# Performance work log

Measured on AMD Instinct MI355X. Metric: run time of the kernel, lower is better.

The kernel has to match this reference:

```python
import jax, jax.numpy as jnp
import numpy as np

N, F, R, E, L = 100000, 128, 4, 1600000, 2


def setup_inputs() -> dict:
    key = jax.random.key(0)
    k1, k2, k3, k4, k5 = jax.random.split(key, 5)
    scale = 1.0 / np.sqrt(F)
    x = jax.random.normal(k1, (N, F), dtype=jnp.float32)
    edge_index = jax.random.randint(k2, (2, E), 0, N, dtype=jnp.int64)
    edge_type = jax.random.randint(k3, (E,), 0, R, dtype=jnp.int64)
    weights = jax.random.normal(k4, (L, R, F, F), dtype=jnp.float32) * scale
    roots = jax.random.normal(k5, (L, F, F), dtype=jnp.float32) * scale
    biases = jnp.zeros((L, F), dtype=jnp.float32)
    return {"x": x, "edge_index": edge_index, "edge_type": edge_type,
            "weights": weights, "roots": roots, "biases": biases}


def _rgcn_layer(x, weight, root, bias, src, dst, etype):
    # weight: [R, F, F]. Transform all nodes by all relation weights: [R, N, F]
    xw = jnp.einsum('nf,rfo->rno', x, weight)
    msgs = xw[etype, src]                       # [E, F] gather per edge
    seg = dst * R + etype                       # combined (node, relation) segment id
    sums = jax.ops.segment_sum(msgs, seg, num_segments=N * R)
    cnt = jax.ops.segment_sum(jnp.ones((msgs.shape[0],), msgs.dtype), seg,
                              num_segments=N * R)
    mean = sums / jnp.maximum(cnt, 1.0)[:, None]  # mean aggregation per relation
    agg = mean.reshape(N, R, F).sum(axis=1)       # sum over relations: [N, F]
    return agg + x @ root + bias


def reference(x, edge_index, edge_type, weights, roots, biases):
    src, dst = edge_index[0], edge_index[1]
    for l in range(L):
        x = _rgcn_layer(x, weights[l], roots[l], biases[l], src, dst, edge_type)
        x = jax.nn.relu(x)  # dropout is identity at eval
    return x
```

## Files before the change

kernel.cpp:

```cpp
#include <hip/hip_runtime.h>
#include <hip/hip_bf16.h>

#define N_NODES 100000
#define FDIM 128
#define RREL 4
#define NEDGE 1600000
#define NSEG (N_NODES * RREL)
#define KB_TOT 20
#define BSW_PER_LAYER (KB_TOT * 8 * 64 * 8)
#define BIN_SHIFT 10
#define BIN_SEGS 1024
#define NBINS ((NSEG + BIN_SEGS - 1) / BIN_SEGS)
#define BIN_CAP 5120
#define EPB 2048
#define SCAT_NB ((NEDGE + EPB - 1) / EPB)
#define CAST_NB ((N_NODES * FDIM / 4) / 256)
#define PREP_NB (2 * BSW_PER_LAYER / 256)
#define CUR_BITS 21

typedef __attribute__((ext_vector_type(8))) short bfrag;
typedef __attribute__((ext_vector_type(4))) float ffrag;
typedef __attribute__((ext_vector_type(2))) float f32x2;

__device__ __forceinline__ unsigned short f2bf(float f) {
    unsigned u = __float_as_uint(f);
    u += 0x7fffu + ((u >> 16) & 1u);
    return (unsigned short)(u >> 16);
}
__device__ __forceinline__ float bf_lo(unsigned u) { return __uint_as_float(u << 16); }
__device__ __forceinline__ float bf_hi(unsigned u) { return __uint_as_float(u & 0xffff0000u); }

__global__ __launch_bounds__(256) void prepA(
    const float* __restrict__ W,
    const float* __restrict__ root,
    unsigned short* __restrict__ Bsw,
    int* __restrict__ binCursor)
{
    int wb = blockIdx.x;
    int idx = wb * 256 + threadIdx.x;
    if (wb < 2) {
        int t = wb * 256 + threadIdx.x;
        if (t < NBINS) binCursor[t] = 0;
    }
    int layer = idx / BSW_PER_LAYER;
    int rem = idx % BSW_PER_LAYER;
    int kb = rem / 4096;
    int rem2 = rem % 4096;
    int ct = rem2 / 512;
    int rem3 = rem2 % 512;
    int lane = rem3 / 8;
    int j = rem3 % 8;
    int k = kb * 32 + (lane >> 4) * 8 + j;
    int n = ct * 16 + (lane & 15);
    float v;
    if (k < 512) v = W[(size_t)layer * 4 * 128 * 128 + (size_t)k * 128 + n];
    else         v = root[(size_t)layer * 128 * 128 + (size_t)(k - 512) * 128 + n];
    Bsw[idx] = f2bf(v);
}

__global__ __launch_bounds__(256) void scatter_cast(
    const int* __restrict__ src, const int* __restrict__ dst,
    const int* __restrict__ et, int* __restrict__ binCursor,
    unsigned* __restrict__ pairs,
    const float* __restrict__ x, unsigned short* __restrict__ xb)
{
    int tid = threadIdx.x;
    if (blockIdx.x >= SCAT_NB) {
        int i = (blockIdx.x - SCAT_NB) * 256 + tid;
        float4 v = ((const float4*)x)[i];
        ushort4 o = { f2bf(v.x), f2bf(v.y), f2bf(v.z), f2bf(v.w) };
        ((ushort4*)xb)[i] = o;
        return;
    }
    __shared__ int hist[NBINS];
    __shared__ int base[NBINS];
    for (int b = tid; b < NBINS; b += 256) hist[b] = 0;
    __syncthreads();
    int e0 = blockIdx.x * EPB;
    int binr[EPB / 256];
    unsigned pkr[EPB / 256];
    #pragma unroll
    for (int i = 0; i < EPB / 256; ++i) {
        int e = e0 + i * 256 + tid;
        if (e < NEDGE) {
            int seg = dst[e] * RREL + et[e];
            binr[i] = seg >> BIN_SHIFT;
            pkr[i] = ((unsigned)src[e] << BIN_SHIFT) | (unsigned)(seg & (BIN_SEGS - 1));
            atomicAdd(&hist[binr[i]], 1);
        } else binr[i] = -1;
    }
    __syncthreads();
    for (int b = tid; b < NBINS; b += 256) {
        int h = hist[b];
        base[b] = h ? atomicAdd(&binCursor[b], h) : 0;
        hist[b] = 0;
    }
    __syncthreads();
    #pragma unroll
    for (int i = 0; i < EPB / 256; ++i) {
        if (binr[i] >= 0) {
            int b = binr[i];
            int li = atomicAdd(&hist[b], 1);
            pairs[(size_t)b * BIN_CAP + base[b] + li] = pkr[i];
        }
    }
}

__global__ __launch_bounds__(1024) void bin_fill(
    const unsigned* __restrict__ pairs, const int* __restrict__ binCursor,
    int* __restrict__ esrc, unsigned* __restrict__ cursorp)
{
    __shared__ int hist[BIN_SEGS];
    __shared__ int cur[BIN_SEGS];
    __shared__ int waveSums[16];
    int b = blockIdx.x;
    int tid = threadIdx.x;
    int seg0 = b << BIN_SHIFT;
    int cnt = binCursor[b];
    size_t pb = (size_t)b * BIN_CAP;
    hist[tid] = 0;
    __syncthreads();
    for (int i = tid; i < cnt; i += 1024)
        atomicAdd(&hist[pairs[pb + i] & (BIN_SEGS - 1)], 1);
    __syncthreads();
    int v = hist[tid];
    int lane = tid & 63, wv = tid >> 6;
    int inc = v;
    #pragma unroll
    for (int d = 1; d < 64; d <<= 1) {
        int o = __shfl_up(inc, d, 64);
        if (lane >= d) inc += o;
    }
    if (lane == 63) waveSums[wv] = inc;
    __syncthreads();
    int wbase = 0;
    for (int w = 0; w < wv; ++w) wbase += waveSums[w];
    int glob = (int)pb + wbase + inc - v;
    int sg = seg0 + tid;
    if (sg < NSEG) cursorp[sg] = (unsigned)glob | ((unsigned)v << CUR_BITS);
    cur[tid] = glob;
    __syncthreads();
    for (int i = tid; i < cnt; i += 1024) {
        unsigned p = pairs[pb + i];
        int pos = atomicAdd(&cur[p & (BIN_SEGS - 1)], 1);
        esrc[pos] = (int)(p >> BIN_SHIFT);
    }
}

__device__ __forceinline__ uint4 ldrow(const unsigned short* xb, int s, int lane16) {
    unsigned off = (unsigned)s * (FDIM * 2) + (unsigned)lane16 * 16u;
    return *(const uint4*)((const char*)xb + off);
}
__device__ __forceinline__ void acc_add(f32x2* acc, uint4 u) {
    f32x2 t0 = {bf_lo(u.x), bf_hi(u.x)}; acc[0] += t0;
    f32x2 t1 = {bf_lo(u.y), bf_hi(u.y)}; acc[1] += t1;
    f32x2 t2 = {bf_lo(u.z), bf_hi(u.z)}; acc[2] += t2;
    f32x2 t3 = {bf_lo(u.w), bf_hi(u.w)}; acc[3] += t3;
}

__global__ __launch_bounds__(256) void rgcn_aggregate(
    const unsigned short* __restrict__ xb, const int* __restrict__ esrc,
    const unsigned* __restrict__ cursorp,
    unsigned short* __restrict__ meanb)
{
    int sub = threadIdx.x >> 4;
    int lane16 = threadIdx.x & 15;
    int seg = blockIdx.x * 16 + sub;
    unsigned cc = cursorp[seg];
    int j = (int)(cc & ((1u << CUR_BITS) - 1u));
    int c = (int)(cc >> CUR_BITS);
    int end = j + c;
    f32x2 acc[4] = {};
    for (; j + 3 < end; j += 4) {
        int s0 = esrc[j], s1 = esrc[j + 1], s2 = esrc[j + 2], s3 = esrc[j + 3];
        uint4 u0 = ldrow(xb, s0, lane16);
        uint4 u1 = ldrow(xb, s1, lane16);
        uint4 u2 = ldrow(xb, s2, lane16);
        uint4 u3 = ldrow(xb, s3, lane16);
        acc_add(acc, u0); acc_add(acc, u1); acc_add(acc, u2); acc_add(acc, u3);
    }
    for (; j < end; ++j) {
        int sv = esrc[j];
        uint4 u = ldrow(xb, sv, lane16);
        acc_add(acc, u);
    }
    float inv = 1.0f / fmaxf((float)c, 1.0f);
    uint4 o;
    o.x = (unsigned)f2bf(acc[0].x * inv) | ((unsigned)f2bf(acc[0].y * inv) << 16);
    o.y = (unsigned)f2bf(acc[1].x * inv) | ((unsigned)f2bf(acc[1].y * inv) << 16);
    o.z = (unsigned)f2bf(acc[2].x * inv) | ((unsigned)f2bf(acc[2].y * inv) << 16);
    o.w = (unsigned)f2bf(acc[3].x * inv) | ((unsigned)f2bf(acc[3].y * inv) << 16);
    ((uint4*)(meanb + (size_t)seg * FDIM))[lane16] = o;
}

__device__ __forceinline__ void gload_lds16(const void* g, void* l) {
    __builtin_amdgcn_global_load_lds(
        (const __attribute__((address_space(1))) unsigned*)g,
        (__attribute__((address_space(3))) unsigned*)l, 16, 0, 0);
}

__global__ __launch_bounds__(256, 3) void rgcn_transform(
    const unsigned short* __restrict__ xb,
    const unsigned short* __restrict__ meanb,
    const unsigned short* __restrict__ Bsw,
    const float* __restrict__ bias,
    float* __restrict__ out,
    unsigned short* __restrict__ xbn,
    const int writeF32)
{
    __shared__ __align__(16) unsigned char Bsm[2][8192];

    int tid = threadIdx.x;
    int wave = tid >> 6, lane = tid & 63;
    int quad = lane >> 4, rlo = lane & 15;
    int n0 = blockIdx.x * 128 + wave * 32;
    int r0 = n0 + rlo;
    int r1 = n0 + 16 + rlo;
    int r0c = min(r0, N_NODES - 1);
    int r1c = min(r1, N_NODES - 1);

    const bfrag* m0 = (const bfrag*)(meanb + (size_t)r0c * 512) + quad;
    const bfrag* m1 = (const bfrag*)(meanb + (size_t)r1c * 512) + quad;
    const bfrag* x0 = (const bfrag*)(xb + (size_t)r0c * FDIM) + quad;
    const bfrag* x1 = (const bfrag*)(xb + (size_t)r1c * FDIM) + quad;

    const char* gBc = (const char*)Bsw;
    #define STAGE_B(kb, buf) do { \
        const char* _g = gBc + (size_t)(kb) * 8192 + tid * 16; \
        char* _l = (char*)Bsm[buf] + wave * 1024; \
        gload_lds16(_g, _l); \
        gload_lds16(_g + 4096, _l + 4096); \
    } while (0)

    #define AFRAG(row, kb) ((kb) < 16 ? row##_m[(kb) * 4] : row##_x[((kb) - 16) * 4])
    const bfrag* r0_m = m0; const bfrag* r0_x = x0;
    const bfrag* r1_m = m1; const bfrag* r1_x = x1;

    ffrag acc[2][8] = {};

    STAGE_B(0, 0);
    bfrag a0p0 = AFRAG(r0, 0), a1p0 = AFRAG(r1, 0);
    bfrag a0p1 = AFRAG(r0, 1), a1p1 = AFRAG(r1, 1);
    __syncthreads();

    #pragma unroll
    for (int kb = 0; kb < KB_TOT; ++kb) {
        int cur = kb & 1;
        if (kb + 1 < KB_TOT) STAGE_B(kb + 1, cur ^ 1);

        bfrag a0 = cur ? a0p1 : a0p0;
        bfrag a1 = cur ? a1p1 : a1p0;
        if (kb + 2 < KB_TOT) {
            if (cur) { a0p1 = AFRAG(r0, kb + 2); a1p1 = AFRAG(r1, kb + 2); }
            else     { a0p0 = AFRAG(r0, kb + 2); a1p0 = AFRAG(r1, kb + 2); }
        }

        #pragma unroll
        for (int ct = 0; ct < 8; ++ct) {
            bfrag b = *(const bfrag*)&Bsm[cur][ct * 1024 + lane * 16];
            acc[0][ct] = __builtin_amdgcn_mfma_f32_16x16x32_bf16(a0, b, acc[0][ct], 0, 0, 0);
            acc[1][ct] = __builtin_amdgcn_mfma_f32_16x16x32_bf16(a1, b, acc[1][ct], 0, 0, 0);
        }
        __syncthreads();
    }
    #undef STAGE_B
    #undef AFRAG

    float bcol[8];
    #pragma unroll
    for (int ct = 0; ct < 8; ++ct) bcol[ct] = bias[ct * 16 + rlo];

    #pragma unroll
    for (int rt = 0; rt < 2; ++rt) {
        int rbase = n0 + rt * 16 + quad * 4;
        #pragma unroll
        for (int i = 0; i < 4; ++i) {
            int r = rbase + i;
            if (r < N_NODES) {
                #pragma unroll
                for (int ct = 0; ct < 8; ++ct) {
                    float v = fmaxf(acc[rt][ct][i] + bcol[ct], 0.0f);
                    int col = ct * 16 + rlo;
                    if (writeF32) out[(size_t)r * FDIM + col] = v;
                    else          xbn[(size_t)r * FDIM + col] = f2bf(v);
                }
            }
        }
    }
}

extern "C" void kernel_launch(void* const* d_in, const int* in_sizes, int n_in,
                              void* d_out, int out_size, void* d_ws, size_t ws_size,
                              hipStream_t stream) {
    const float* x        = (const float*)d_in[0];
    const int* edge_index = (const int*)d_in[1];
    const int* edge_type  = (const int*)d_in[2];
    const float* weights  = (const float*)d_in[3];
    const float* roots    = (const float*)d_in[4];
    const float* biases   = (const float*)d_in[5];
    float* out = (float*)d_out;

    unsigned short* meanb = (unsigned short*)d_ws;
    unsigned* pairs = (unsigned*)d_ws;
    unsigned short* xb0   = meanb + (size_t)NSEG * FDIM;
    unsigned short* xb1   = xb0 + (size_t)N_NODES * FDIM;
    unsigned short* Bsw   = xb1 + (size_t)N_NODES * FDIM;
    int* esrc   = (int*)(Bsw + 2 * BSW_PER_LAYER);
    unsigned* cursorp = (unsigned*)(esrc + (size_t)NBINS * BIN_CAP);
    int* binCursor = (int*)(cursorp + NSEG);

    const int* src = edge_index;
    const int* dst = edge_index + NEDGE;

    prepA<<<PREP_NB, 256, 0, stream>>>(weights, roots, Bsw, binCursor);
    scatter_cast<<<SCAT_NB + CAST_NB, 256, 0, stream>>>(src, dst, edge_type,
                                                        binCursor, pairs, x, xb0);
    bin_fill<<<NBINS, 1024, 0, stream>>>(pairs, binCursor, esrc, cursorp);

    const int tgrid = (N_NODES + 127) / 128;

    rgcn_aggregate<<<NSEG / 16, 256, 0, stream>>>(xb0, esrc, cursorp, meanb);
    rgcn_transform<<<tgrid, 256, 0, stream>>>(xb0, meanb, Bsw, biases, out, xb1, 0);
    rgcn_aggregate<<<NSEG / 16, 256, 0, stream>>>(xb1, esrc, cursorp, meanb);
    rgcn_transform<<<tgrid, 256, 0, stream>>>(xb1, meanb, Bsw + BSW_PER_LAYER,
                                              biases + FDIM, out, xb0, 1);
}
```

Baseline: 366.0 us.

## Merge weight prep into scatter kernel and double B-stage depth per barrier

Folds the weight-swizzle prep into the scatter/cast launch and replaces the cursor-zeroing done in prepA with a memset. In the transform kernel, each pipeline stage now loads two K-blocks of B (16KB per buffer) so there are half as many barriers per tile. The cost is double the LDS footprint per block, which may limit occupancy under the 3-blocks-per-CU launch bound.

```diff
diff --git a/kernel.cpp b/kernel.cpp
--- a/kernel.cpp
+++ b/kernel.cpp
@@ -7,6 +7,7 @@
 #define NEDGE 1600000
 #define NSEG (N_NODES * RREL)
 #define KB_TOT 20
+#define NSTAGE 10
 #define BSW_PER_LAYER (KB_TOT * 8 * 64 * 8)
 #define BIN_SHIFT 10
 #define BIN_SEGS 1024
@@ -30,46 +31,40 @@
 __device__ __forceinline__ float bf_lo(unsigned u) { return __uint_as_float(u << 16); }
 __device__ __forceinline__ float bf_hi(unsigned u) { return __uint_as_float(u & 0xffff0000u); }
 
-__global__ __launch_bounds__(256) void prepA(
-    const float* __restrict__ W,
-    const float* __restrict__ root,
-    unsigned short* __restrict__ Bsw,
-    int* __restrict__ binCursor)
-{
-    int wb = blockIdx.x;
-    int idx = wb * 256 + threadIdx.x;
-    if (wb < 2) {
-        int t = wb * 256 + threadIdx.x;
-        if (t < NBINS) binCursor[t] = 0;
-    }
-    int layer = idx / BSW_PER_LAYER;
-    int rem = idx % BSW_PER_LAYER;
-    int kb = rem / 4096;
-    int rem2 = rem % 4096;
-    int ct = rem2 / 512;
-    int rem3 = rem2 % 512;
-    int lane = rem3 / 8;
-    int j = rem3 % 8;
-    int k = kb * 32 + (lane >> 4) * 8 + j;
-    int n = ct * 16 + (lane & 15);
-    float v;
-    if (k < 512) v = W[(size_t)layer * 4 * 128 * 128 + (size_t)k * 128 + n];
-    else         v = root[(size_t)layer * 128 * 128 + (size_t)(k - 512) * 128 + n];
-    Bsw[idx] = f2bf(v);
-}
-
-__global__ __launch_bounds__(256) void scatter_cast(
+__global__ __launch_bounds__(256) void scatter_cast_prep(
     const int* __restrict__ src, const int* __restrict__ dst,
     const int* __restrict__ et, int* __restrict__ binCursor,
     unsigned* __restrict__ pairs,
-    const float* __restrict__ x, unsigned short* __restrict__ xb)
+    const float* __restrict__ x, unsigned short* __restrict__ xb,
+    const float* __restrict__ W,
+    const float* __restrict__ root,
+    unsigned short* __restrict__ Bsw)
 {
     int tid = threadIdx.x;
     if (blockIdx.x >= SCAT_NB) {
-        int i = (blockIdx.x - SCAT_NB) * 256 + tid;
-        float4 v = ((const float4*)x)[i];
-        ushort4 o = { f2bf(v.x), f2bf(v.y), f2bf(v.z), f2bf(v.w) };
-        ((ushort4*)xb)[i] = o;
+        int t = blockIdx.x - SCAT_NB;
+        if (t < CAST_NB) {
+            int i = t * 256 + tid;
+            float4 v = ((const float4*)x)[i];
+            ushort4 o = { f2bf(v.x), f2bf(v.y), f2bf(v.z), f2bf(v.w) };
+            ((ushort4*)xb)[i] = o;
+        } else {
+            int idx = (t - CAST_NB) * 256 + tid;
+            int layer = idx / BSW_PER_LAYER;
+            int rem = idx % BSW_PER_LAYER;
+            int kb = rem / 4096;
+            int rem2 = rem % 4096;
+            int ct = rem2 / 512;
+            int rem3 = rem2 % 512;
+            int lane = rem3 / 8;
+            int j = rem3 % 8;
+            int k = kb * 32 + (lane >> 4) * 8 + j;
+            int n = ct * 16 + (lane & 15);
+            float v;
+            if (k < 512) v = W[(size_t)layer * 4 * 128 * 128 + (size_t)k * 128 + n];
+            else         v = root[(size_t)layer * 128 * 128 + (size_t)(k - 512) * 128 + n];
+            Bsw[idx] = f2bf(v);
+        }
         return;
     }
     __shared__ int hist[NBINS];
@@ -208,16 +203,14 @@
     unsigned short* __restrict__ xbn,
     const int writeF32)
 {
-    __shared__ __align__(16) unsigned char Bsm[2][8192];
+    __shared__ __align__(16) unsigned char Bsm[2][16384];
 
     int tid = threadIdx.x;
     int wave = tid >> 6, lane = tid & 63;
     int quad = lane >> 4, rlo = lane & 15;
     int n0 = blockIdx.x * 128 + wave * 32;
-    int r0 = n0 + rlo;
-    int r1 = n0 + 16 + rlo;
-    int r0c = min(r0, N_NODES - 1);
-    int r1c = min(r1, N_NODES - 1);
+    int r0c = min(n0 + rlo, N_NODES - 1);
+    int r1c = min(n0 + 16 + rlo, N_NODES - 1);
 
     const bfrag* m0 = (const bfrag*)(meanb + (size_t)r0c * 512) + quad;
     const bfrag* m1 = (const bfrag*)(meanb + (size_t)r1c * 512) + quad;
@@ -225,11 +218,13 @@
     const bfrag* x1 = (const bfrag*)(xb + (size_t)r1c * FDIM) + quad;
 
     const char* gBc = (const char*)Bsw;
-    #define STAGE_B(kb, buf) do { \
-        const char* _g = gBc + (size_t)(kb) * 8192 + tid * 16; \
+    #define STAGE_B(st, buf) do { \
+        const char* _g = gBc + (size_t)(st) * 16384 + tid * 16; \
         char* _l = (char*)Bsm[buf] + wave * 1024; \
         gload_lds16(_g, _l); \
         gload_lds16(_g + 4096, _l + 4096); \
+        gload_lds16(_g + 8192, _l + 8192); \
+        gload_lds16(_g + 12288, _l + 12288); \
     } while (0)
 
     #define AFRAG(row, kb) ((kb) < 16 ? row##_m[(kb) * 4] : row##_x[((kb) - 16) * 4])
@@ -239,28 +234,32 @@
     ffrag acc[2][8] = {};
 
     STAGE_B(0, 0);
-    bfrag a0p0 = AFRAG(r0, 0), a1p0 = AFRAG(r1, 0);
-    bfrag a0p1 = AFRAG(r0, 1), a1p1 = AFRAG(r1, 1);
-    __syncthreads();
-
-    #pragma unroll
-    for (int kb = 0; kb < KB_TOT; ++kb) {
-        int cur = kb & 1;
-        if (kb + 1 < KB_TOT) STAGE_B(kb + 1, cur ^ 1);
-
-        bfrag a0 = cur ? a0p1 : a0p0;
-        bfrag a1 = cur ? a1p1 : a1p0;
-        if (kb + 2 < KB_TOT) {
-            if (cur) { a0p1 = AFRAG(r0, kb + 2); a1p1 = AFRAG(r1, kb + 2); }
-            else     { a0p0 = AFRAG(r0, kb + 2); a1p0 = AFRAG(r1, kb + 2); }
-        }
-
+    bfrag a00 = AFRAG(r0, 0), a10 = AFRAG(r1, 0);
+    bfrag a01 = AFRAG(r0, 1), a11 = AFRAG(r1, 1);
+    __syncthreads();
+
+    #pragma unroll
+    for (int st = 0; st < NSTAGE; ++st) {
+        int cur = st & 1;
+        bfrag n00 = a00, n10 = a10, n01 = a01, n11 = a11;
+        if (st + 1 < NSTAGE) {
+            STAGE_B(st + 1, cur ^ 1);
+            n00 = AFRAG(r0, 2 * st + 2); n10 = AFRAG(r1, 2 * st + 2);
+            n01 = AFRAG(r0, 2 * st + 3); n11 = AFRAG(r1, 2 * st + 3);
+        }
         #pragma unroll
         for (int ct = 0; ct < 8; ++ct) {
             bfrag b = *(const bfrag*)&Bsm[cur][ct * 1024 + lane * 16];
-            acc[0][ct] = __builtin_amdgcn_mfma_f32_16x16x32_bf16(a0, b, acc[0][ct], 0, 0, 0);
-            acc[1][ct] = __builtin_amdgcn_mfma_f32_16x16x32_bf16(a1, b, acc[1][ct], 0, 0, 0);
-        }
+            acc[0][ct] = __builtin_amdgcn_mfma_f32_16x16x32_bf16(a00, b, acc[0][ct], 0, 0, 0);
+            acc[1][ct] = __builtin_amdgcn_mfma_f32_16x16x32_bf16(a10, b, acc[1][ct], 0, 0, 0);
+        }
+        #pragma unroll
+        for (int ct = 0; ct < 8; ++ct) {
+            bfrag b = *(const bfrag*)&Bsm[cur][8192 + ct * 1024 + lane * 16];
+            acc[0][ct] = __builtin_amdgcn_mfma_f32_16x16x32_bf16(a01, b, acc[0][ct], 0, 0, 0);
+            acc[1][ct] = __builtin_amdgcn_mfma_f32_16x16x32_bf16(a11, b, acc[1][ct], 0, 0, 0);
+        }
+        a00 = n00; a10 = n10; a01 = n01; a11 = n11;
         __syncthreads();
     }
     #undef STAGE_B
@@ -312,9 +311,9 @@
     const int* src = edge_index;
     const int* dst = edge_index + NEDGE;
 
-    prepA<<<PREP_NB, 256, 0, stream>>>(weights, roots, Bsw, binCursor);
-    scatter_cast<<<SCAT_NB + CAST_NB, 256, 0, stream>>>(src, dst, edge_type,
-                                                        binCursor, pairs, x, xb0);
+    hipMemsetAsync(binCursor, 0, NBINS * sizeof(int), stream);
+    scatter_cast_prep<<<SCAT_NB + CAST_NB + PREP_NB, 256, 0, stream>>>(
+        src, dst, edge_type, binCursor, pairs, x, xb0, weights, roots, Bsw);
     bin_fill<<<NBINS, 1024, 0, stream>>>(pairs, binCursor, esrc, cursorp);
 
     const int tgrid = (N_NODES + 127) / 128;
```

Result: no change. 368.5 us (+0.7%).
